# Kernel optimization log

Measured on AMD Instinct MI355X. Metric: run time of the kernel, lower is better.

The kernel has to match this reference:

```python
import jax, jax.numpy as jnp
import numpy as np

N_NODES = 50000
N_EDGES = 800000
F_IN = 64
HID = 64
N_CLASSES = 10
NUM_LAYERS = 3


def setup_inputs() -> dict:
    key = jax.random.key(0)
    ks = jax.random.split(key, 10)
    x = jax.random.normal(ks[0], (N_NODES, F_IN), dtype=jnp.float32)
    edge_index = jax.random.randint(ks[1], (2, N_EDGES), 0, N_NODES, dtype=jnp.int64)
    edge_weight = jax.random.uniform(ks[2], (N_EDGES,), dtype=jnp.float32)
    # layer weights: [F_IN->HID, HID->HID, HID->N_CLASSES]
    s0 = 1.0 / np.sqrt(F_IN)
    s1 = 1.0 / np.sqrt(HID)
    W0 = jax.random.uniform(ks[3], (F_IN, HID), jnp.float32, -s0, s0)
    b0 = jnp.zeros((HID,), jnp.float32)
    W1 = jax.random.uniform(ks[4], (HID, HID), jnp.float32, -s1, s1)
    b1 = jnp.zeros((HID,), jnp.float32)
    W2 = jax.random.uniform(ks[5], (HID, N_CLASSES), jnp.float32, -s1, s1)
    b2 = jnp.zeros((N_CLASSES,), jnp.float32)
    return {"x": x, "edge_index": edge_index, "edge_weight": edge_weight,
            "W0": W0, "b0": b0, "W1": W1, "b1": b1, "W2": W2, "b2": b2}


def _gcn_layer(h, W, b, src, dst, ew):
    # linear transform then weighted sum-aggregation over incoming edges
    h = h @ W                                   # [N, d_out]
    msg = h[src] * ew[:, None]                  # gather + scale  [E, d_out]
    agg = jax.ops.segment_sum(msg, dst, num_segments=N_NODES)  # scatter-add
    return agg + b


def reference(x, edge_index, edge_weight, W0, b0, W1, b1, W2, b2):
    src, dst = edge_index[0], edge_index[1]
    h = _gcn_layer(x, W0, b0, src, dst, edge_weight)
    h = jax.nn.softmax(h, axis=-1)              # act='softmax' between layers
    h = _gcn_layer(h, W1, b1, src, dst, edge_weight)
    h = jax.nn.softmax(h, axis=-1)
    h = _gcn_layer(h, W2, b2, src, dst, edge_weight)  # final layer, no act
    return jax.nn.softmax(h, axis=-1)           # wrapper F.softmax(dim=-1)
```

## Files before the change

### kernel.cpp

```cpp
#include <hip/hip_runtime.h>
#include <hip/hip_fp16.h>

#define NN 50000
#define NE 800000
#define NBUCK 196
#define P1_EDGES 4096
#define P2_CAP 6144

__global__ __launch_bounds__(256) void cast16_kernel(const float* __restrict__ x,
                                                     __half* __restrict__ x16) {
    int i = blockIdx.x * 256 + threadIdx.x;
    if (i < NN * 32) {
        float2 v = reinterpret_cast<const float2*>(x)[i];
        reinterpret_cast<__half2*>(x16)[i] = __floats2half2_rn(v.x, v.y);
    }
}

__global__ __launch_bounds__(256) void count_kernel(const int* __restrict__ dst,
                                                    int* __restrict__ cnt) {
    int e = blockIdx.x * 256 + threadIdx.x;
    if (e < NE) atomicAdd(&cnt[dst[e]], 1);
}

__global__ __launch_bounds__(256) void scan1_kernel(const int* __restrict__ cnt,
                                                    int* __restrict__ offs,
                                                    int* __restrict__ bsum) {
    __shared__ int sm[256];
    int b = blockIdx.x, t = threadIdx.x;
    int base = b * 2048 + t * 8;
    int v[8];
    int s = 0;
#pragma unroll
    for (int i = 0; i < 8; ++i) {
        int idx = base + i;
        int c = (idx < NN) ? cnt[idx] : 0;
        v[i] = s;
        s += c;
    }
    sm[t] = s;
    __syncthreads();
    for (int off = 1; off < 256; off <<= 1) {
        int y = (t >= off) ? sm[t - off] : 0;
        __syncthreads();
        sm[t] += y;
        __syncthreads();
    }
    int excl = sm[t] - s;
#pragma unroll
    for (int i = 0; i < 8; ++i) {
        int idx = base + i;
        if (idx < NN) offs[idx] = excl + v[i];
    }
    if (t == 255) bsum[b] = sm[255];
}

__global__ __launch_bounds__(256) void scan3_kernel(int* __restrict__ offs,
                                                    const int* __restrict__ bsum,
                                                    int* __restrict__ gcursor) {
    __shared__ int sb[32];
    if (threadIdx.x == 0) {
        int run = 0;
        for (int k = 0; k < 25; ++k) {
            sb[k] = run;
            run += bsum[k];
        }
    }
    __syncthreads();
    int i = blockIdx.x * 256 + threadIdx.x;
    if (i < NN) {
        int v = offs[i] + sb[i >> 11];
        offs[i] = v;
        if ((i & 255) == 0) gcursor[i >> 8] = v;
    }
    if (i == 0) offs[NN] = NE;
}

__global__ __launch_bounds__(256) void sortp1_kernel(const int* __restrict__ src,
                                                     const int* __restrict__ dst,
                                                     const float* __restrict__ ew,
                                                     int* __restrict__ gcursor,
                                                     int2* __restrict__ epairT) {
    __shared__ int hist[256];
    __shared__ int binBase[256];
    __shared__ int gBase[256];
    __shared__ int scanTmp[256];
    __shared__ int2 buf[P1_EDGES];
    __shared__ unsigned char bb[P1_EDGES];
    int tid = threadIdx.x;
    int e0 = blockIdx.x * P1_EDGES;
    int total = NE - e0;
    if (total > P1_EDGES) total = P1_EDGES;

    hist[tid] = 0;
    __syncthreads();
    for (int r = 0; r < 16; ++r) {
        int e = e0 + r * 256 + tid;
        if (e < NE) atomicAdd(&hist[dst[e] >> 8], 1);
    }
    __syncthreads();
    int v = hist[tid];
    scanTmp[tid] = v;
    __syncthreads();
    for (int off = 1; off < 256; off <<= 1) {
        int y = (tid >= off) ? scanTmp[tid - off] : 0;
        __syncthreads();
        scanTmp[tid] += y;
        __syncthreads();
    }
    int excl = scanTmp[tid] - v;
    binBase[tid] = excl;
    hist[tid] = excl;
    __syncthreads();
    for (int r = 0; r < 16; ++r) {
        int e = e0 + r * 256 + tid;
        if (e < NE) {
            int d = dst[e];
            int bk = d >> 8;
            int slot = atomicAdd(&hist[bk], 1);
            buf[slot] = make_int2(src[e] | ((d & 255) << 16), __float_as_int(ew[e]));
            bb[slot] = (unsigned char)bk;
        }
    }
    __syncthreads();
    int c = hist[tid] - binBase[tid];
    gBase[tid] = (c > 0) ? atomicAdd(&gcursor[tid], c) : 0;
    __syncthreads();
    for (int i = tid; i < total; i += 256) {
        int bk = bb[i];
        epairT[gBase[bk] + (i - binBase[bk])] = buf[i];
    }
}

__global__ __launch_bounds__(256) void sortp2_kernel(const int2* __restrict__ epairT,
                                                     const int* __restrict__ offs,
                                                     int2* __restrict__ epair) {
    __shared__ int hist[256];
    __shared__ int scanTmp[256];
    __shared__ int2 buf[P2_CAP];
    int tid = threadIdx.x;
    int b = blockIdx.x;
    int n0 = b << 8;
    int nEnd = n0 + 256;
    if (nEnd > NN) nEnd = NN;
    int base = offs[n0];
    int total = offs[nEnd] - base;

    hist[tid] = 0;
    __syncthreads();
    for (int i = tid; i < total; i += 256) {
        int2 q = epairT[base + i];
        atomicAdd(&hist[(q.x >> 16) & 255], 1);
    }
    __syncthreads();
    int v = hist[tid];
    scanTmp[tid] = v;
    __syncthreads();
    for (int off = 1; off < 256; off <<= 1) {
        int y = (tid >= off) ? scanTmp[tid - off] : 0;
        __syncthreads();
        scanTmp[tid] += y;
        __syncthreads();
    }
    hist[tid] = scanTmp[tid] - v;
    __syncthreads();
    for (int i = tid; i < total; i += 256) {
        int2 q = epairT[base + i];
        int slot = atomicAdd(&hist[(q.x >> 16) & 255], 1);
        buf[slot] = make_int2(q.x & 0xFFFF, q.y);
    }
    __syncthreads();
    for (int i = tid; i < total; i += 256) epair[base + i] = buf[i];
}

__global__ __launch_bounds__(256) void fused4_kernel(const __half* __restrict__ h,
                                                     const int* __restrict__ offs,
                                                     const int2* __restrict__ epair,
                                                     const float* __restrict__ W,
                                                     const float* __restrict__ b,
                                                     __half* __restrict__ out) {
    __shared__ float Wl[4096];
    int tid = threadIdx.x;
    for (int i = tid; i < 1024; i += 256)
        reinterpret_cast<float4*>(Wl)[i] = reinterpret_cast<const float4*>(W)[i];
    __syncthreads();

    int lane = tid & 63;
    int wid = (blockIdx.x * 256 + tid) >> 6;
    int n0 = wid * 4;
    if (n0 >= NN) return;

    float av[4];
#pragma unroll
    for (int m = 0; m < 4; ++m) {
        int n = n0 + m;
        int beg = __builtin_amdgcn_readfirstlane(offs[n]);
        int end = __builtin_amdgcn_readfirstlane(offs[n + 1]);
        float a = 0.f;
        int i = beg;
        for (; i + 7 < end; i += 8) {
            int2 q0 = epair[i + 0], q1 = epair[i + 1], q2 = epair[i + 2], q3 = epair[i + 3];
            int2 q4 = epair[i + 4], q5 = epair[i + 5], q6 = epair[i + 6], q7 = epair[i + 7];
            int s0 = __builtin_amdgcn_readfirstlane(q0.x);
            int s1 = __builtin_amdgcn_readfirstlane(q1.x);
            int s2 = __builtin_amdgcn_readfirstlane(q2.x);
            int s3 = __builtin_amdgcn_readfirstlane(q3.x);
            int s4 = __builtin_amdgcn_readfirstlane(q4.x);
            int s5 = __builtin_amdgcn_readfirstlane(q5.x);
            int s6 = __builtin_amdgcn_readfirstlane(q6.x);
            int s7 = __builtin_amdgcn_readfirstlane(q7.x);
            float h0 = __half2float(h[((size_t)s0 << 6) + lane]);
            float h1 = __half2float(h[((size_t)s1 << 6) + lane]);
            float h2 = __half2float(h[((size_t)s2 << 6) + lane]);
            float h3 = __half2float(h[((size_t)s3 << 6) + lane]);
            float h4 = __half2float(h[((size_t)s4 << 6) + lane]);
            float h5 = __half2float(h[((size_t)s5 << 6) + lane]);
            float h6 = __half2float(h[((size_t)s6 << 6) + lane]);
            float h7 = __half2float(h[((size_t)s7 << 6) + lane]);
            a = fmaf(h0, __int_as_float(__builtin_amdgcn_readfirstlane(q0.y)), a);
            a = fmaf(h1, __int_as_float(__builtin_amdgcn_readfirstlane(q1.y)), a);
            a = fmaf(h2, __int_as_float(__builtin_amdgcn_readfirstlane(q2.y)), a);
            a = fmaf(h3, __int_as_float(__builtin_amdgcn_readfirstlane(q3.y)), a);
            a = fmaf(h4, __int_as_float(__builtin_amdgcn_readfirstlane(q4.y)), a);
            a = fmaf(h5, __int_as_float(__builtin_amdgcn_readfirstlane(q5.y)), a);
            a = fmaf(h6, __int_as_float(__builtin_amdgcn_readfirstlane(q6.y)), a);
            a = fmaf(h7, __int_as_float(__builtin_amdgcn_readfirstlane(q7.y)), a);
        }
        for (; i < end; ++i) {
            int2 q = epair[i];
            int s = __builtin_amdgcn_readfirstlane(q.x);
            float w = __int_as_float(__builtin_amdgcn_readfirstlane(q.y));
            a = fmaf(__half2float(h[((size_t)s << 6) + lane]), w, a);
        }
        av[m] = a;
    }

    int i0 = __float_as_int(av[0]), i1 = __float_as_int(av[1]);
    int i2 = __float_as_int(av[2]), i3 = __float_as_int(av[3]);
    float y0 = 0.f, y1 = 0.f, y2 = 0.f, y3 = 0.f;
#pragma unroll
    for (int k = 0; k < 64; ++k) {
        float w = Wl[k * 64 + lane];
        y0 = fmaf(__int_as_float(__builtin_amdgcn_readlane(i0, k)), w, y0);
        y1 = fmaf(__int_as_float(__builtin_amdgcn_readlane(i1, k)), w, y1);
        y2 = fmaf(__int_as_float(__builtin_amdgcn_readlane(i2, k)), w, y2);
        y3 = fmaf(__int_as_float(__builtin_amdgcn_readlane(i3, k)), w, y3);
    }
    float bl = b[lane];
    y0 += bl; y1 += bl; y2 += bl; y3 += bl;

#pragma unroll
    for (int m = 0; m < 4; ++m) {
        float y = (m == 0) ? y0 : (m == 1) ? y1 : (m == 2) ? y2 : y3;
        float mx = y;
#pragma unroll
        for (int o = 32; o; o >>= 1) mx = fmaxf(mx, __shfl_xor(mx, o, 64));
        float p = __expf(y - mx);
        float s2 = p;
#pragma unroll
        for (int o = 32; o; o >>= 1) s2 += __shfl_xor(s2, o, 64);
        out[(size_t)(n0 + m) * 64 + lane] = __float2half_rn(p / s2);
    }
}

__global__ __launch_bounds__(256) void lin16h_kernel(const __half* __restrict__ H,
                                                     const float* __restrict__ W2,
                                                     __half* __restrict__ out) {
    int g = blockIdx.x * 256 + threadIdx.x;
    int n = g >> 4, j = g & 15;
    if (n >= NN) return;
    float acc = 0.f;
    if (j < 10) {
        const __half* hrow = H + (size_t)n * 64;
#pragma unroll
        for (int k = 0; k < 64; ++k) acc += __half2float(hrow[k]) * W2[k * 10 + j];
    }
    out[(size_t)n * 16 + j] = __float2half_rn(acc);
}

__global__ __launch_bounds__(256) void aggsm10h_kernel(const __half* __restrict__ u2,
                                                       const int* __restrict__ offs,
                                                       const int2* __restrict__ epair,
                                                       const float* __restrict__ b,
                                                       float* __restrict__ out) {
    int g = blockIdx.x * 256 + threadIdx.x;
    int n = g >> 4, j = g & 15;
    if (n >= NN) return;
    int beg = offs[n], end = offs[n + 1];
    float acc = 0.f;
    int i = beg;
    for (; i + 3 < end; i += 4) {
        int2 p0 = epair[i], p1 = epair[i + 1], p2 = epair[i + 2], p3 = epair[i + 3];
        float h0 = __half2float(u2[(size_t)p0.x * 16 + j]);
        float h1 = __half2float(u2[(size_t)p1.x * 16 + j]);
        float h2 = __half2float(u2[(size_t)p2.x * 16 + j]);
        float h3 = __half2float(u2[(size_t)p3.x * 16 + j]);
        acc = fmaf(h0, __int_as_float(p0.y), acc);
        acc = fmaf(h1, __int_as_float(p1.y), acc);
        acc = fmaf(h2, __int_as_float(p2.y), acc);
        acc = fmaf(h3, __int_as_float(p3.y), acc);
    }
    for (; i < end; ++i) {
        int2 p0 = epair[i];
        acc = fmaf(__half2float(u2[(size_t)p0.x * 16 + j]), __int_as_float(p0.y), acc);
    }
    float v = (j < 10) ? (acc + b[j]) : -1e30f;
    float m = v;
#pragma unroll
    for (int o = 8; o; o >>= 1) m = fmaxf(m, __shfl_xor(m, o, 64));
    float p = (j < 10) ? __expf(v - m) : 0.f;
    float s2 = p;
#pragma unroll
    for (int o = 8; o; o >>= 1) s2 += __shfl_xor(s2, o, 64);
    if (j < 10) out[(size_t)n * 10 + j] = p / s2;
}

extern "C" void kernel_launch(void* const* d_in, const int* in_sizes, int n_in,
                              void* d_out, int out_size, void* d_ws, size_t ws_size,
                              hipStream_t stream) {
    const float* x  = (const float*)d_in[0];
    const int*   ei = (const int*)d_in[1];
    const float* ew = (const float*)d_in[2];
    const float* W0 = (const float*)d_in[3];
    const float* b0 = (const float*)d_in[4];
    const float* W1 = (const float*)d_in[5];
    const float* b1 = (const float*)d_in[6];
    const float* W2 = (const float*)d_in[7];
    const float* b2 = (const float*)d_in[8];
    float* out = (float*)d_out;

    const int* src = ei;
    const int* dst = ei + NE;

    char* ws = (char*)d_ws;
    const size_t SZH = (size_t)NN * 64 * sizeof(__half);
    __half* X16   = (__half*)ws;
    __half* H1    = (__half*)(ws + SZH);
    __half* H2    = (__half*)(ws + 2 * SZH);
    __half* U     = (__half*)(ws + 3 * SZH);
    int2*  epair  = (int2*)(ws + 3 * SZH + (size_t)NN * 16 * 2);
    int2*  epairT = (int2*)(ws + 3 * SZH + (size_t)NN * 16 * 2 + (size_t)NE * 8);
    char*  tail   = ws + 3 * SZH + (size_t)NN * 16 * 2 + 2 * (size_t)NE * 8;
    int*   offs    = (int*)tail;
    int*   cnt     = offs + (NN + 1);
    int*   bsum    = cnt + NN;
    int*   gcursor = bsum + 32;

    const int gE   = (NE + 255) / 256;
    const int gN   = (NN + 255) / 256;
    const int gC   = (NN * 32 + 255) / 256;
    const int gF4  = (NN * 16 + 255) / 256;
    const int gN16 = (NN * 16 + 255) / 256;
    const int gP1  = (NE + P1_EDGES - 1) / P1_EDGES;

    hipMemsetAsync(cnt, 0, (size_t)NN * sizeof(int), stream);
    cast16_kernel<<<gC, 256, 0, stream>>>(x, X16);
    count_kernel<<<gE, 256, 0, stream>>>(dst, cnt);
    scan1_kernel<<<25, 256, 0, stream>>>(cnt, offs, bsum);
    scan3_kernel<<<gN, 256, 0, stream>>>(offs, bsum, gcursor);
    sortp1_kernel<<<gP1, 256, 0, stream>>>(src, dst, ew, gcursor, epairT);
    sortp2_kernel<<<NBUCK, 256, 0, stream>>>(epairT, offs, epair);

    fused4_kernel<<<gF4, 256, 0, stream>>>(X16, offs, epair, W0, b0, H1);

    fused4_kernel<<<gF4, 256, 0, stream>>>(H1, offs, epair, W1, b1, H2);

    lin16h_kernel<<<gN16, 256, 0, stream>>>(H2, W2, U);

    aggsm10h_kernel<<<gN16, 256, 0, stream>>>(U, offs, epair, b2, out);
}
```

Measured before the change: 264.3 us.

## Count per bucket only, derive CSR offsets in sort pass, pack edges to 32-bit

Replaces the per-node atomic count and the two-level scan with a shared-memory histogram over 196 buckets and a single-block scan. Per-node CSR offsets are now produced inside the second sort pass from its local histogram. Each edge record is packed into one 32-bit word (16-bit source index plus fp16 weight), halving the edge stream read by the three aggregation kernels. Storing the weight in fp16 loses precision, and the 16-bit source field depends on the node count staying below 65536.

Result: faster. 223.3 us (-15.5%).

```diff
diff --git a/kernel.cpp b/kernel.cpp
--- a/kernel.cpp
+++ b/kernel.cpp
@@ -16,28 +16,29 @@
     }
 }
 
-__global__ __launch_bounds__(256) void count_kernel(const int* __restrict__ dst,
-                                                    int* __restrict__ cnt) {
-    int e = blockIdx.x * 256 + threadIdx.x;
-    if (e < NE) atomicAdd(&cnt[dst[e]], 1);
-}
-
-__global__ __launch_bounds__(256) void scan1_kernel(const int* __restrict__ cnt,
-                                                    int* __restrict__ offs,
-                                                    int* __restrict__ bsum) {
+__global__ __launch_bounds__(256) void countB_kernel(const int* __restrict__ dst,
+                                                     int* __restrict__ gcnt) {
+    __shared__ int hist[256];
+    int tid = threadIdx.x;
+    hist[tid] = 0;
+    __syncthreads();
+    int e0 = blockIdx.x * P1_EDGES;
+    for (int r = 0; r < 16; ++r) {
+        int e = e0 + r * 256 + tid;
+        if (e < NE) atomicAdd(&hist[dst[e] >> 8], 1);
+    }
+    __syncthreads();
+    int c = hist[tid];
+    if (c) atomicAdd(&gcnt[tid], c);
+}
+
+__global__ __launch_bounds__(256) void scanB_kernel(const int* __restrict__ gcnt,
+                                                    int* __restrict__ gbase,
+                                                    int* __restrict__ gcursor) {
     __shared__ int sm[256];
-    int b = blockIdx.x, t = threadIdx.x;
-    int base = b * 2048 + t * 8;
-    int v[8];
-    int s = 0;
-#pragma unroll
-    for (int i = 0; i < 8; ++i) {
-        int idx = base + i;
-        int c = (idx < NN) ? cnt[idx] : 0;
-        v[i] = s;
-        s += c;
-    }
-    sm[t] = s;
+    int t = threadIdx.x;
+    int v = (t < NBUCK) ? gcnt[t] : 0;
+    sm[t] = v;
     __syncthreads();
     for (int off = 1; off < 256; off <<= 1) {
         int y = (t >= off) ? sm[t - off] : 0;
@@ -45,34 +46,12 @@
         sm[t] += y;
         __syncthreads();
     }
-    int excl = sm[t] - s;
-#pragma unroll
-    for (int i = 0; i < 8; ++i) {
-        int idx = base + i;
-        if (idx < NN) offs[idx] = excl + v[i];
-    }
-    if (t == 255) bsum[b] = sm[255];
-}
-
-__global__ __launch_bounds__(256) void scan3_kernel(int* __restrict__ offs,
-                                                    const int* __restrict__ bsum,
-                                                    int* __restrict__ gcursor) {
-    __shared__ int sb[32];
-    if (threadIdx.x == 0) {
-        int run = 0;
-        for (int k = 0; k < 25; ++k) {
-            sb[k] = run;
-            run += bsum[k];
-        }
-    }
-    __syncthreads();
-    int i = blockIdx.x * 256 + threadIdx.x;
-    if (i < NN) {
-        int v = offs[i] + sb[i >> 11];
-        offs[i] = v;
-        if ((i & 255) == 0) gcursor[i >> 8] = v;
-    }
-    if (i == 0) offs[NN] = NE;
+    int excl = sm[t] - v;
+    if (t < NBUCK) {
+        gbase[t] = excl;
+        gcursor[t] = excl;
+    }
+    if (t == 0) gbase[NBUCK] = NE;
 }
 
 __global__ __launch_bounds__(256) void sortp1_kernel(const int* __restrict__ src,
@@ -132,18 +111,16 @@
 }
 
 __global__ __launch_bounds__(256) void sortp2_kernel(const int2* __restrict__ epairT,
-                                                     const int* __restrict__ offs,
-                                                     int2* __restrict__ epair) {
+                                                     const int* __restrict__ gbase,
+                                                     int* __restrict__ offs,
+                                                     int* __restrict__ epair) {
     __shared__ int hist[256];
     __shared__ int scanTmp[256];
-    __shared__ int2 buf[P2_CAP];
+    __shared__ int buf[P2_CAP];
     int tid = threadIdx.x;
     int b = blockIdx.x;
-    int n0 = b << 8;
-    int nEnd = n0 + 256;
-    if (nEnd > NN) nEnd = NN;
-    int base = offs[n0];
-    int total = offs[nEnd] - base;
+    int base = gbase[b];
+    int total = gbase[b + 1] - base;
 
     hist[tid] = 0;
     __syncthreads();
@@ -161,12 +138,17 @@
         scanTmp[tid] += y;
         __syncthreads();
     }
-    hist[tid] = scanTmp[tid] - v;
+    int excl = scanTmp[tid] - v;
+    int n = (b << 8) + tid;
+    if (n < NN) offs[n] = base + excl;
+    if (b == NBUCK - 1 && tid == 0) offs[NN] = NE;
+    hist[tid] = excl;
     __syncthreads();
     for (int i = tid; i < total; i += 256) {
         int2 q = epairT[base + i];
         int slot = atomicAdd(&hist[(q.x >> 16) & 255], 1);
-        buf[slot] = make_int2(q.x & 0xFFFF, q.y);
+        unsigned short wh = __half_as_ushort(__float2half_rn(__int_as_float(q.y)));
+        buf[slot] = (q.x & 0xFFFF) | ((int)wh << 16);
     }
     __syncthreads();
     for (int i = tid; i < total; i += 256) epair[base + i] = buf[i];
@@ -174,7 +156,7 @@
 
 __global__ __launch_bounds__(256) void fused4_kernel(const __half* __restrict__ h,
                                                      const int* __restrict__ offs,
-                                                     const int2* __restrict__ epair,
+                                                     const int* __restrict__ epair,
                                                      const float* __restrict__ W,
                                                      const float* __restrict__ b,
                                                      __half* __restrict__ out) {
@@ -198,38 +180,35 @@
         float a = 0.f;
         int i = beg;
         for (; i + 7 < end; i += 8) {
-            int2 q0 = epair[i + 0], q1 = epair[i + 1], q2 = epair[i + 2], q3 = epair[i + 3];
-            int2 q4 = epair[i + 4], q5 = epair[i + 5], q6 = epair[i + 6], q7 = epair[i + 7];
-            int s0 = __builtin_amdgcn_readfirstlane(q0.x);
-            int s1 = __builtin_amdgcn_readfirstlane(q1.x);
-            int s2 = __builtin_amdgcn_readfirstlane(q2.x);
-            int s3 = __builtin_amdgcn_readfirstlane(q3.x);
-            int s4 = __builtin_amdgcn_readfirstlane(q4.x);
-            int s5 = __builtin_amdgcn_readfirstlane(q5.x);
-            int s6 = __builtin_amdgcn_readfirstlane(q6.x);
-            int s7 = __builtin_amdgcn_readfirstlane(q7.x);
-            float h0 = __half2float(h[((size_t)s0 << 6) + lane]);
-            float h1 = __half2float(h[((size_t)s1 << 6) + lane]);
-            float h2 = __half2float(h[((size_t)s2 << 6) + lane]);
-            float h3 = __half2float(h[((size_t)s3 << 6) + lane]);
-            float h4 = __half2float(h[((size_t)s4 << 6) + lane]);
-            float h5 = __half2float(h[((size_t)s5 << 6) + lane]);
-            float h6 = __half2float(h[((size_t)s6 << 6) + lane]);
-            float h7 = __half2float(h[((size_t)s7 << 6) + lane]);
-            a = fmaf(h0, __int_as_float(__builtin_amdgcn_readfirstlane(q0.y)), a);
-            a = fmaf(h1, __int_as_float(__builtin_amdgcn_readfirstlane(q1.y)), a);
-            a = fmaf(h2, __int_as_float(__builtin_amdgcn_readfirstlane(q2.y)), a);
-            a = fmaf(h3, __int_as_float(__builtin_amdgcn_readfirstlane(q3.y)), a);
-            a = fmaf(h4, __int_as_float(__builtin_amdgcn_readfirstlane(q4.y)), a);
-            a = fmaf(h5, __int_as_float(__builtin_amdgcn_readfirstlane(q5.y)), a);
-            a = fmaf(h6, __int_as_float(__builtin_amdgcn_readfirstlane(q6.y)), a);
-            a = fmaf(h7, __int_as_float(__builtin_amdgcn_readfirstlane(q7.y)), a);
+            int u0 = __builtin_amdgcn_readfirstlane(epair[i + 0]);
+            int u1 = __builtin_amdgcn_readfirstlane(epair[i + 1]);
+            int u2 = __builtin_amdgcn_readfirstlane(epair[i + 2]);
+            int u3 = __builtin_amdgcn_readfirstlane(epair[i + 3]);
+            int u4 = __builtin_amdgcn_readfirstlane(epair[i + 4]);
+            int u5 = __builtin_amdgcn_readfirstlane(epair[i + 5]);
+            int u6 = __builtin_amdgcn_readfirstlane(epair[i + 6]);
+            int u7 = __builtin_amdgcn_readfirstlane(epair[i + 7]);
+            float h0 = __half2float(h[((size_t)(u0 & 0xFFFF) << 6) + lane]);
+            float h1 = __half2float(h[((size_t)(u1 & 0xFFFF) << 6) + lane]);
+            float h2 = __half2float(h[((size_t)(u2 & 0xFFFF) << 6) + lane]);
+            float h3 = __half2float(h[((size_t)(u3 & 0xFFFF) << 6) + lane]);
+            float h4 = __half2float(h[((size_t)(u4 & 0xFFFF) << 6) + lane]);
+            float h5 = __half2float(h[((size_t)(u5 & 0xFFFF) << 6) + lane]);
+            float h6 = __half2float(h[((size_t)(u6 & 0xFFFF) << 6) + lane]);
+            float h7 = __half2float(h[((size_t)(u7 & 0xFFFF) << 6) + lane]);
+            a = fmaf(h0, __half2float(__ushort_as_half((unsigned short)(u0 >> 16))), a);
+            a = fmaf(h1, __half2float(__ushort_as_half((unsigned short)(u1 >> 16))), a);
+            a = fmaf(h2, __half2float(__ushort_as_half((unsigned short)(u2 >> 16))), a);
+            a = fmaf(h3, __half2float(__ushort_as_half((unsigned short)(u3 >> 16))), a);
+            a = fmaf(h4, __half2float(__ushort_as_half((unsigned short)(u4 >> 16))), a);
+            a = fmaf(h5, __half2float(__ushort_as_half((unsigned short)(u5 >> 16))), a);
+            a = fmaf(h6, __half2float(__ushort_as_half((unsigned short)(u6 >> 16))), a);
+            a = fmaf(h7, __half2float(__ushort_as_half((unsigned short)(u7 >> 16))), a);
         }
         for (; i < end; ++i) {
-            int2 q = epair[i];
-            int s = __builtin_amdgcn_readfirstlane(q.x);
-            float w = __int_as_float(__builtin_amdgcn_readfirstlane(q.y));
-            a = fmaf(__half2float(h[((size_t)s << 6) + lane]), w, a);
+            int u = __builtin_amdgcn_readfirstlane(epair[i]);
+            float hw = __half2float(__ushort_as_half((unsigned short)(u >> 16)));
+            a = fmaf(__half2float(h[((size_t)(u & 0xFFFF) << 6) + lane]), hw, a);
         }
         av[m] = a;
     }
@@ -279,7 +258,7 @@
 
 __global__ __launch_bounds__(256) void aggsm10h_kernel(const __half* __restrict__ u2,
                                                        const int* __restrict__ offs,
-                                                       const int2* __restrict__ epair,
+                                                       const int* __restrict__ epair,
                                                        const float* __restrict__ b,
                                                        float* __restrict__ out) {
     int g = blockIdx.x * 256 + threadIdx.x;
@@ -289,19 +268,20 @@
     float acc = 0.f;
     int i = beg;
     for (; i + 3 < end; i += 4) {
-        int2 p0 = epair[i], p1 = epair[i + 1], p2 = epair[i + 2], p3 = epair[i + 3];
-        float h0 = __half2float(u2[(size_t)p0.x * 16 + j]);
-        float h1 = __half2float(u2[(size_t)p1.x * 16 + j]);
-        float h2 = __half2float(u2[(size_t)p2.x * 16 + j]);
-        float h3 = __half2float(u2[(size_t)p3.x * 16 + j]);
-        acc = fmaf(h0, __int_as_float(p0.y), acc);
-        acc = fmaf(h1, __int_as_float(p1.y), acc);
-        acc = fmaf(h2, __int_as_float(p2.y), acc);
-        acc = fmaf(h3, __int_as_float(p3.y), acc);
+        int q0 = epair[i], q1 = epair[i + 1], q2 = epair[i + 2], q3 = epair[i + 3];
+        float h0 = __half2float(u2[(size_t)(q0 & 0xFFFF) * 16 + j]);
+        float h1 = __half2float(u2[(size_t)(q1 & 0xFFFF) * 16 + j]);
+        float h2 = __half2float(u2[(size_t)(q2 & 0xFFFF) * 16 + j]);
+        float h3 = __half2float(u2[(size_t)(q3 & 0xFFFF) * 16 + j]);
+        acc = fmaf(h0, __half2float(__ushort_as_half((unsigned short)(q0 >> 16))), acc);
+        acc = fmaf(h1, __half2float(__ushort_as_half((unsigned short)(q1 >> 16))), acc);
+        acc = fmaf(h2, __half2float(__ushort_as_half((unsigned short)(q2 >> 16))), acc);
+        acc = fmaf(h3, __half2float(__ushort_as_half((unsigned short)(q3 >> 16))), acc);
     }
     for (; i < end; ++i) {
-        int2 p0 = epair[i];
-        acc = fmaf(__half2float(u2[(size_t)p0.x * 16 + j]), __int_as_float(p0.y), acc);
+        int q = epair[i];
+        acc = fmaf(__half2float(u2[(size_t)(q & 0xFFFF) * 16 + j]),
+                   __half2float(__ushort_as_half((unsigned short)(q >> 16))), acc);
     }
     float v = (j < 10) ? (acc + b[j]) : -1e30f;
     float m = v;
@@ -337,28 +317,25 @@
     __half* H1    = (__half*)(ws + SZH);
     __half* H2    = (__half*)(ws + 2 * SZH);
     __half* U     = (__half*)(ws + 3 * SZH);
-    int2*  epair  = (int2*)(ws + 3 * SZH + (size_t)NN * 16 * 2);
-    int2*  epairT = (int2*)(ws + 3 * SZH + (size_t)NN * 16 * 2 + (size_t)NE * 8);
-    char*  tail   = ws + 3 * SZH + (size_t)NN * 16 * 2 + 2 * (size_t)NE * 8;
+    int*   epair  = (int*)(ws + 3 * SZH + (size_t)NN * 16 * 2);
+    int2*  epairT = (int2*)(ws + 3 * SZH + (size_t)NN * 16 * 2 + (size_t)NE * 4);
+    char*  tail   = ws + 3 * SZH + (size_t)NN * 16 * 2 + (size_t)NE * 4 + (size_t)NE * 8;
     int*   offs    = (int*)tail;
-    int*   cnt     = offs + (NN + 1);
-    int*   bsum    = cnt + NN;
-    int*   gcursor = bsum + 32;
-
-    const int gE   = (NE + 255) / 256;
-    const int gN   = (NN + 255) / 256;
+    int*   gcnt    = offs + (NN + 1);
+    int*   gbase   = gcnt + 256;
+    int*   gcursor = gbase + (NBUCK + 1);
+
     const int gC   = (NN * 32 + 255) / 256;
     const int gF4  = (NN * 16 + 255) / 256;
     const int gN16 = (NN * 16 + 255) / 256;
     const int gP1  = (NE + P1_EDGES - 1) / P1_EDGES;
 
-    hipMemsetAsync(cnt, 0, (size_t)NN * sizeof(int), stream);
+    hipMemsetAsync(gcnt, 0, 256 * sizeof(int), stream);
     cast16_kernel<<<gC, 256, 0, stream>>>(x, X16);
-    count_kernel<<<gE, 256, 0, stream>>>(dst, cnt);
-    scan1_kernel<<<25, 256, 0, stream>>>(cnt, offs, bsum);
-    scan3_kernel<<<gN, 256, 0, stream>>>(offs, bsum, gcursor);
+    countB_kernel<<<gP1, 256, 0, stream>>>(dst, gcnt);
+    scanB_kernel<<<1, 256, 0, stream>>>(gcnt, gbase, gcursor);
     sortp1_kernel<<<gP1, 256, 0, stream>>>(src, dst, ew, gcursor, epairT);
-    sortp2_kernel<<<NBUCK, 256, 0, stream>>>(epairT, offs, epair);
+    sortp2_kernel<<<NBUCK, 256, 0, stream>>>(epairT, gbase, offs, epair);
 
     fused4_kernel<<<gF4, 256, 0, stream>>>(X16, offs, epair, W0, b0, H1);
 
```
